# Kernel tuning notes

Hardware: AMD Instinct MI355X
Metric: run time of the kernel (lower is better)

## Reference

```python
import jax, jax.numpy as jnp
import numpy as np

NUM_EVENTS = 8   # events per batch (equal-sized, so we can reshape [N] -> [B,E])
K = 16           # kNN neighbors (includes self, distance 0 -> weight 1)
LN_EPS = 1e-5


def setup_inputs() -> dict:
    key = jax.random.key(0)
    ks = jax.random.split(key, 4)
    N, D, S, P = 32768, 256, 4, 32
    x = jax.random.normal(ks[0], (N, D), jnp.float32)
    batch_index = jnp.repeat(jnp.arange(NUM_EVENTS, dtype=jnp.int32), N // NUM_EVENTS)
    def lin(k, fan_in, fan_out):
        return jax.random.normal(k, (fan_in, fan_out), jnp.float32) / np.sqrt(fan_in).astype(np.float32)
    Ws = lin(ks[1], D, S);            bs = jnp.zeros((S,), jnp.float32)
    Wh = lin(ks[2], D, P);            bh = jnp.zeros((P,), jnp.float32)
    Wo = lin(ks[3], D + 2 * P, D);    bo = jnp.zeros((D,), jnp.float32)
    gamma = jnp.ones((D,), jnp.float32)
    beta = jnp.zeros((D,), jnp.float32)
    return dict(x=x, batch_index=batch_index, Ws=Ws, bs=bs, Wh=Wh, bh=bh,
                Wo=Wo, bo=bo, gamma=gamma, beta=beta)


def reference(x, batch_index, Ws, bs, Wh, bh, Wo, bo, gamma, beta):
    # GravNetConv: learned-space kNN + distance-weighted mean/max aggregation,
    # followed by residual add + LayerNorm (dropout p=0, eval mode).
    N, D = x.shape
    B = NUM_EVENTS
    E = N // B                                   # equal-sized events (batch_index is block-sorted)
    s = (x @ Ws + bs).reshape(B, E, -1)          # [B,E,S] learned coordinates
    h = (x @ Wh + bh).reshape(B, E, -1)          # [B,E,P] propagated features
    # per-event squared distances [B,E,E]; S=4 so this is traffic-bound
    d2 = jnp.sum((s[:, :, None, :] - s[:, None, :, :]) ** 2, axis=-1)
    neg_d2_k, idx = jax.lax.top_k(-d2, K)        # k smallest distances; idx [B,E,K]
    w = jnp.exp(10.0 * neg_d2_k)                 # edge_weight = exp(-10 * d^2), [B,E,K]
    h_nb = jax.vmap(lambda hb, ib: hb[ib])(h, idx)   # gather neighbor feats [B,E,K,P]
    msg = h_nb * w[..., None]                    # weighted messages
    agg_mean = jnp.mean(msg, axis=2)             # [B,E,P]
    agg_max = jnp.max(msg, axis=2)               # [B,E,P]
    xb = x.reshape(B, E, D)
    x_new = jnp.concatenate([xb, agg_mean, agg_max], axis=-1) @ Wo + bo  # lin_out
    # residual + LayerNorm
    y = xb + x_new
    mu = jnp.mean(y, axis=-1, keepdims=True)
    var = jnp.mean((y - mu) ** 2, axis=-1, keepdims=True)
    y = gamma * (y - mu) * jax.lax.rsqrt(var + LN_EPS) + beta
    return y.reshape(N, D)
```

## Files before the change

### kernel.cpp

```cpp
#include <hip/hip_runtime.h>
#include <stdint.h>

typedef short short8 __attribute__((ext_vector_type(8)));
typedef float f32x4 __attribute__((ext_vector_type(4)));
typedef unsigned short u16;

#define N_TOT 32768
#define EV 4096

__device__ __forceinline__ u16 f2bf(float f){
  unsigned int x = __float_as_uint(f);
  x += 0x7FFFu + ((x >> 16) & 1u);
  return (u16)(x >> 16);
}
__device__ __forceinline__ unsigned umin_(unsigned a, unsigned b){ return a<b?a:b; }

__global__ __launch_bounds__(256, 3) void kA(
    const float* __restrict__ x, const float* __restrict__ Ws,
    const float* __restrict__ bs, const float* __restrict__ Wh,
    const float* __restrict__ bh, const float* __restrict__ Wo,
    float* __restrict__ sOut, uint4* __restrict__ sfrag,
    unsigned short* __restrict__ hOut, unsigned int* __restrict__ WoT2)
{
  if (blockIdx.x >= N_TOT/64){
    const int kb = (blockIdx.x - N_TOT/64) * 32;
    const int c = threadIdx.x;
    unsigned int prev = 0;
    for (int k=0;k<32;++k){
      float v = Wo[(size_t)(kb+k)*256 + c];
      u16 h = f2bf(v);
      if (k & 1) WoT2[(size_t)c*160 + ((kb+k)>>1)] = prev | ((unsigned)h<<16);
      else       prev = (unsigned)h;
    }
    return;
  }
  __shared__ u16 xh[64*264];
  __shared__ u16 whT[32*264];
  const int t = threadIdx.x;
  const int wv = t >> 6, l = t & 63;
  const int r0 = blockIdx.x * 64;

  #pragma unroll
  for (int i=0;i<32;++i){
    int k = i*8 + (t>>5);
    int col = t & 31;
    whT[col*264 + k] = f2bf(Wh[(size_t)k*32 + col]);
  }

  {
    const int row = t >> 2, c40 = t & 3;
    const float4* xr = (const float4*)(x + (size_t)(r0+row)*256);
    const float4* wsr = (const float4*)Ws;
    float a0=0.f,a1=0.f,a2=0.f,a3=0.f;
    #pragma unroll
    for (int i=0;i<16;++i){
      int c4 = c40 + i*4;
      float4 xv = xr[c4];
      unsigned p0,p1;
      asm("v_cvt_pk_bf16_f32 %0, %1, %2" : "=v"(p0) : "v"(xv.x), "v"(xv.y));
      asm("v_cvt_pk_bf16_f32 %0, %1, %2" : "=v"(p1) : "v"(xv.z), "v"(xv.w));
      uint2 pk = {p0, p1};
      *(uint2*)&xh[row*264 + c4*4] = pk;
      float4 w0 = wsr[c4*4+0], w1 = wsr[c4*4+1], w2 = wsr[c4*4+2], w3 = wsr[c4*4+3];
      a0 += xv.x*w0.x + xv.y*w1.x + xv.z*w2.x + xv.w*w3.x;
      a1 += xv.x*w0.y + xv.y*w1.y + xv.z*w2.y + xv.w*w3.y;
      a2 += xv.x*w0.z + xv.y*w1.z + xv.z*w2.z + xv.w*w3.z;
      a3 += xv.x*w0.w + xv.y*w1.w + xv.z*w2.w + xv.w*w3.w;
    }
    a0 += __shfl_xor(a0,1); a0 += __shfl_xor(a0,2);
    a1 += __shfl_xor(a1,1); a1 += __shfl_xor(a1,2);
    a2 += __shfl_xor(a2,1); a2 += __shfl_xor(a2,2);
    a3 += __shfl_xor(a3,1); a3 += __shfl_xor(a3,2);
    if (c40 == 0){
      float4 sv = { a0+bs[0], a1+bs[1], a2+bs[2], a3+bs[3] };
      ((float4*)sOut)[r0 + row] = sv;
      u16 h0=f2bf(sv.x), h1=f2bf(sv.y), h2=f2bf(sv.z), h3=f2bf(sv.w);
      float e0 = sv.x - __uint_as_float((unsigned)h0<<16);
      float e1 = sv.y - __uint_as_float((unsigned)h1<<16);
      float e2 = sv.z - __uint_as_float((unsigned)h2<<16);
      float e3 = sv.w - __uint_as_float((unsigned)h3<<16);
      u16 l0=f2bf(e0), l1=f2bf(e1), l2=f2bf(e2), l3=f2bf(e3);
      float n = sv.x*sv.x + sv.y*sv.y + sv.z*sv.z + sv.w*sv.w;
      u16 nh = f2bf(n);
      u16 nl = f2bf(n - __uint_as_float((unsigned)nh<<16));
      uint4 w0, w1;
      w0.x = (unsigned)h0 | ((unsigned)h1<<16);
      w0.y = (unsigned)h2 | ((unsigned)h3<<16);
      w0.z = w0.x; w0.w = w0.y;
      w1.x = (unsigned)l0 | ((unsigned)l1<<16);
      w1.y = (unsigned)l2 | ((unsigned)l3<<16);
      w1.z = (unsigned)nh | ((unsigned)nl<<16);
      w1.w = 0x3F803F80u;
      sfrag[(size_t)(r0+row)*2 + 0] = w0;
      sfrag[(size_t)(r0+row)*2 + 1] = w1;
    }
  }
  __syncthreads();

  {
    const int lq = l & 15, g = l >> 4;
    const f32x4 zero = {0.f,0.f,0.f,0.f};
    f32x4 h0 = zero, h1 = zero;
    #pragma unroll
    for (int ks=0; ks<8; ++ks){
      short8 a  = *(const short8*)&xh[(wv*16+lq)*264 + ks*32 + g*8];
      short8 b0 = *(const short8*)&whT[lq*264       + ks*32 + g*8];
      short8 b1 = *(const short8*)&whT[(16+lq)*264  + ks*32 + g*8];
      h0 = __builtin_amdgcn_mfma_f32_16x16x32_bf16(a, b0, h0, 0,0,0);
      h1 = __builtin_amdgcn_mfma_f32_16x16x32_bf16(a, b1, h1, 0,0,0);
    }
    float bv0 = bh[lq], bv1 = bh[16+lq];
    #pragma unroll
    for (int rg=0; rg<4; ++rg){
      int rowg = r0 + wv*16 + g*4 + rg;
      hOut[(size_t)rowg*32 + lq]      = f2bf(h0[rg] + bv0);
      hOut[(size_t)rowg*32 + 16 + lq] = f2bf(h1[rg] + bv1);
    }
  }
}

#define BUBBLE16(v)                                              \
  { _Pragma("unroll")                                            \
    for (int k=0;k<16;++k){                                      \
      unsigned int mn = (v) < bp[k] ? (v) : bp[k];               \
      unsigned int mx = (v) < bp[k] ? bp[k] : (v);               \
      bp[k] = mn; (v) = mx;                                      \
    } }

#define MERGE16(OT)                                              \
  { unsigned int c[16];                                          \
    _Pragma("unroll")                                            \
    for (int k=0;k<16;++k){ unsigned int b2 = (OT)[15-k];        \
      c[k] = bp[k] < b2 ? bp[k] : b2; }                          \
    _Pragma("unroll")                                            \
    for (int d=8; d>=1; d>>=1){                                  \
      _Pragma("unroll")                                          \
      for (int i=0;i<16;++i){                                    \
        if ((i & d) == 0){                                       \
          unsigned int lo = c[i] < c[i+d] ? c[i] : c[i+d];       \
          unsigned int hi = c[i] < c[i+d] ? c[i+d] : c[i];       \
          c[i] = lo; c[i+d] = hi;                                \
        }                                                        \
      }                                                          \
    }                                                            \
    _Pragma("unroll")                                            \
    for (int k=0;k<16;++k) bp[k] = c[k]; }

#define SCAP 448
#define BIN_LO 440u

#define P1BODY(F, TL)                                            \
  { union { uint4 q; short8 v; } au; au.q = (F);                 \
    if (ld) (F) = fw[(size_t)((TL)+4)*32 + a32];                 \
    f32x4 acc = __builtin_amdgcn_mfma_f32_16x16x32_bf16(au.v, bq, zacc, 0,0,0); \
    _Pragma("unroll")                                            \
    for (int rg=0; rg<4; ++rg){                                  \
      unsigned u = __float_as_uint(fmaxf(acc[rg],0.f));          \
      unsigned q21 = u >> 21;                                    \
      unsigned b = (q21 < BIN_LO) ? 0u : umin_(q21 - BIN_LO, 127u); \
      atomicAdd(&hist[hbase + (b>>1)], (b&1u) ? 0x10000u : 1u);  \
    } }

#define P2BODY(F, TL)                                            \
  { union { uint4 q; short8 v; } au; au.q = (F);                 \
    if (ld) (F) = fw[(size_t)((TL)+4)*32 + a32];                 \
    f32x4 acc = __builtin_amdgcn_mfma_f32_16x16x32_bf16(au.v, bq, zacc, 0,0,0); \
    const int jb = jt + (TL)*16;                                 \
    _Pragma("unroll")                                            \
    for (int rg=0; rg<4; ++rg){                                  \
      int u = (int)__float_as_uint(acc[rg]);                     \
      if (u < tauS){                                             \
        unsigned idx = atomicAdd(&scnt[q16], 1u);                \
        if (idx < (unsigned)SCAP) slist[q16*SCAP + idx] = (u16)(jb + rg); \
      }                                                          \
    } }

__global__ __launch_bounds__(256, 8) void kB(
    const float* __restrict__ sIn, const uint4* __restrict__ sfrag,
    const unsigned short* __restrict__ hIn, unsigned short* __restrict__ Umini)
{
  __shared__ unsigned int hist[16*65];
  __shared__ u16 slist[16*SCAP];
  __shared__ unsigned int scnt[16];
  __shared__ unsigned int tauL[16];
  __shared__ unsigned int mrg[48][17];
  const int t = threadIdx.x;
  const int wv = t >> 6, l = t & 63;
  const int e = blockIdx.x >> 8;
  const int qblk = (blockIdx.x & 255) * 16;
  const int q16 = l & 15, g = l >> 4;
  const int qloc = qblk + q16;

  const float4* sg = (const float4*)sIn;
  const float4 sq = sg[(size_t)e*EV + qloc];
  const float si2 = sq.x*sq.x + sq.y*sq.y + sq.z*sq.z + sq.w*sq.w;

  union BU { u16 u[8]; short8 v; } bu;
  #pragma unroll
  for (int i2=0;i2<8;++i2) bu.u[i2]=0;
  {
    float tx=-2.f*sq.x, ty=-2.f*sq.y, tz=-2.f*sq.z, tw=-2.f*sq.w;
    u16 h0=f2bf(tx), h1=f2bf(ty), h2=f2bf(tz), h3=f2bf(tw);
    if (g==0){
      float e0 = tx - __uint_as_float((unsigned)h0<<16);
      float e1 = ty - __uint_as_float((unsigned)h1<<16);
      float e2 = tz - __uint_as_float((unsigned)h2<<16);
      float e3 = tw - __uint_as_float((unsigned)h3<<16);
      bu.u[0]=h0; bu.u[1]=h1; bu.u[2]=h2; bu.u[3]=h3;
      bu.u[4]=f2bf(e0); bu.u[5]=f2bf(e1); bu.u[6]=f2bf(e2); bu.u[7]=f2bf(e3);
    } else if (g==1){
      u16 sh = f2bf(si2);
      u16 sl = f2bf(si2 - __uint_as_float((unsigned)sh<<16));
      bu.u[0]=h0; bu.u[1]=h1; bu.u[2]=h2; bu.u[3]=h3;
      bu.u[4]=0x3F80; bu.u[5]=0x3F80; bu.u[6]=sh; bu.u[7]=sl;
    }
  }
  const short8 bq = bu.v;

  for (int i=t; i<16*65; i+=256) hist[i]=0;
  if (t < 16) scnt[t] = 0;
  __syncthreads();

  const f32x4 zacc = {0.f,0.f,0.f,0.f};
  const uint4 zf4 = {0,0,0,0};
  const uint4* fw = sfrag + (((size_t)e*EV + wv*1024) << 1);
  const int a32 = q16*2 + g;
  const bool ld = (l < 32);
  const int hbase = q16*65;

  {
    uint4 f0 = ld ? fw[a32]      : zf4;
    uint4 f1 = ld ? fw[32 + a32] : zf4;
    uint4 f2 = ld ? fw[64 + a32] : zf4;
    uint4 f3 = ld ? fw[96 + a32] : zf4;
    for (int tl=0; tl<16; tl+=4){
      P1BODY(f0, tl+0)
      P1BODY(f1, tl+1)
      P1BODY(f2, tl+2)
      P1BODY(f3, tl+3)
    }
  }
  __syncthreads();

  {
    int q = t >> 4, i = t & 15;
    int base = q*65 + i*4;
    unsigned w0=hist[base], w1=hist[base+1], w2=hist[base+2], w3=hist[base+3];
    unsigned cnt[8] = { w0&0xFFFFu, w0>>16, w1&0xFFFFu, w1>>16,
                        w2&0xFFFFu, w2>>16, w3&0xFFFFu, w3>>16 };
    unsigned cs = 0;
    #pragma unroll
    for (int k2=0;k2<8;++k2) cs += cnt[k2];
    unsigned ps = cs;
    #pragma unroll
    for (int d=1; d<16; d<<=1){
      unsigned o = __shfl_up(ps, d, 16);
      if ((t&15) >= d) ps += o;
    }
    if (ps >= 16u && (ps - cs) < 16u){
      unsigned run = ps - cs;
      unsigned B = 127;
      #pragma unroll
      for (int k2=0;k2<8;++k2){
        unsigned c2 = cnt[k2];
        bool hit = (run < 16u) && (run + c2 >= 16u);
        if (hit) B = (unsigned)(i*8 + k2);
        run += c2;
      }
      tauL[q] = (B >= 127u) ? 0x7F800001u : ((BIN_LO + B + 1u) << 21);
    }
  }
  __syncthreads();
  const int tauS = (int)tauL[q16];

  {
    uint4 f0 = ld ? fw[a32]      : zf4;
    uint4 f1 = ld ? fw[32 + a32] : zf4;
    uint4 f2 = ld ? fw[64 + a32] : zf4;
    uint4 f3 = ld ? fw[96 + a32] : zf4;
    const int jt = wv*1024 + g*4;
    for (int tl=0; tl<64; tl+=4){
      P2BODY(f0, tl+0)
      P2BODY(f1, tl+1)
      P2BODY(f2, tl+2)
      P2BODY(f3, tl+3)
    }
  }
  __syncthreads();

  unsigned scn_raw = scnt[q16];
  unsigned int bp[16];
  #pragma unroll
  for (int k=0;k<16;++k) bp[k]=0xFFFFFFFFu;
  const int lane16 = wv*4 + g;
  if (scn_raw > (unsigned)SCAP){
    for (int jj=lane16; jj<EV; jj+=16){
      float4 s4 = sg[(size_t)e*EV + jj];
      float dx = sq.x-s4.x, dy = sq.y-s4.y, dz = sq.z-s4.z, dw = sq.w-s4.w;
      float d2 = dx*dx + dy*dy + dz*dz + dw*dw;
      unsigned key = (__float_as_uint(d2) & 0xFFFFF000u) | (unsigned)jj;
      if (key < bp[15]) { BUBBLE16(key) }
    }
  } else {
    for (unsigned i=lane16; i<scn_raw; i+=16){
      int jj = (int)slist[q16*SCAP + i];
      float4 s4 = sg[(size_t)e*EV + jj];
      float dx = sq.x-s4.x, dy = sq.y-s4.y, dz = sq.z-s4.z, dw = sq.w-s4.w;
      float d2 = dx*dx + dy*dy + dz*dz + dw*dw;
      unsigned key = (__float_as_uint(d2) & 0xFFFFF000u) | (unsigned)jj;
      BUBBLE16(key)
    }
  }

  #pragma unroll
  for (int st=0; st<2; ++st){
    const int msk = (st==0) ? 16 : 32;
    unsigned int ot[16];
    #pragma unroll
    for (int k=0;k<16;++k) ot[k] = (unsigned int)__shfl_xor((int)bp[k], msk, 64);
    MERGE16(ot)
  }

  if (wv != 0 && l < 16){
    #pragma unroll
    for (int k=0;k<16;++k) mrg[(wv-1)*16 + l][k] = bp[k];
  }
  __syncthreads();
  if (wv != 0) return;
  #pragma unroll
  for (int w=0; w<3; ++w){
    unsigned int ot[16];
    #pragma unroll
    for (int k=0;k<16;++k) ot[k] = mrg[w*16 + q16][k];
    MERGE16(ot)
  }

  float am[8], ax[8];
  #pragma unroll
  for (int p=0;p<8;++p){ am[p]=0.f; ax[p]=-3.4e38f; }
  const uint4* hb = (const uint4*)(hIn + (size_t)e*EV*32);
  #pragma unroll
  for (int i=0;i<16;++i){
    unsigned int key = bp[i];
    int j = (int)(key & 0xFFFu);
    float d2 = __uint_as_float(key & 0xFFFFF000u);
    float w = __expf(-10.f * d2);
    uint4 hv = hb[(size_t)j*4 + g];
    unsigned int uu[4] = {hv.x, hv.y, hv.z, hv.w};
    #pragma unroll
    for (int c2=0;c2<4;++c2){
      float flo = __uint_as_float(uu[c2] << 16);
      float fhi = __uint_as_float(uu[c2] & 0xFFFF0000u);
      float m0 = w*flo, m1 = w*fhi;
      am[c2*2]   += m0;                 am[c2*2+1] += m1;
      ax[c2*2]    = fmaxf(ax[c2*2],m0); ax[c2*2+1]  = fmaxf(ax[c2*2+1],m1);
    }
  }
  {
    unsigned short* Ur = Umini + ((size_t)e*EV + qloc)*64;
    uint4 pm, px;
    pm.x = (unsigned)f2bf(am[0]*(1.f/16.f)) | ((unsigned)f2bf(am[1]*(1.f/16.f))<<16);
    pm.y = (unsigned)f2bf(am[2]*(1.f/16.f)) | ((unsigned)f2bf(am[3]*(1.f/16.f))<<16);
    pm.z = (unsigned)f2bf(am[4]*(1.f/16.f)) | ((unsigned)f2bf(am[5]*(1.f/16.f))<<16);
    pm.w = (unsigned)f2bf(am[6]*(1.f/16.f)) | ((unsigned)f2bf(am[7]*(1.f/16.f))<<16);
    px.x = (unsigned)f2bf(ax[0]) | ((unsigned)f2bf(ax[1])<<16);
    px.y = (unsigned)f2bf(ax[2]) | ((unsigned)f2bf(ax[3])<<16);
    px.z = (unsigned)f2bf(ax[4]) | ((unsigned)f2bf(ax[5])<<16);
    px.w = (unsigned)f2bf(ax[6]) | ((unsigned)f2bf(ax[7])<<16);
    *(uint4*)(Ur +  0 + g*8) = pm;
    *(uint4*)(Ur + 32 + g*8) = px;
  }
}

__global__ __launch_bounds__(256, 4) void kC(
    const unsigned short* __restrict__ Umini, const unsigned short* __restrict__ WoT,
    const float* __restrict__ bo, const float* __restrict__ x,
    const float* __restrict__ gamma, const float* __restrict__ beta,
    float* __restrict__ out)
{
  __shared__ unsigned short At[64*40];
  __shared__ unsigned short Bt[256*40];
  __shared__ float ps[64*4], pq[64*4];
  const int t = threadIdx.x;
  const int r0 = blockIdx.x * 64;
  const int l = t & 63, wv = t >> 6;
  const int lq = l & 15, g = l >> 4;
  f32x4 acc[4][4];
  const f32x4 zero = {0.f,0.f,0.f,0.f};
  #pragma unroll
  for (int m=0;m<4;++m)
    #pragma unroll
    for (int n=0;n<4;++n) acc[m][n] = zero;

  for (int kk=0; kk<10; ++kk){
    const int k0 = kk*32;
    __syncthreads();
    {
      int row = t >> 2, ko = (t & 3)*8;
      uint4 av;
      if (k0 < 256){
        const float4* xr = (const float4*)(x + (size_t)(r0+row)*256 + k0 + ko);
        float4 u0 = xr[0], u1 = xr[1];
        unsigned p0,p1,p2,p3;
        asm("v_cvt_pk_bf16_f32 %0, %1, %2" : "=v"(p0) : "v"(u0.x), "v"(u0.y));
        asm("v_cvt_pk_bf16_f32 %0, %1, %2" : "=v"(p1) : "v"(u0.z), "v"(u0.w));
        asm("v_cvt_pk_bf16_f32 %0, %1, %2" : "=v"(p2) : "v"(u1.x), "v"(u1.y));
        asm("v_cvt_pk_bf16_f32 %0, %1, %2" : "=v"(p3) : "v"(u1.z), "v"(u1.w));
        av.x = p0; av.y = p1; av.z = p2; av.w = p3;
      } else {
        av = *(const uint4*)(Umini + (size_t)(r0+row)*64 + (k0-256) + ko);
      }
      *(uint4*)(At + row*40 + ko) = av;
    }
    {
      int col = t;
      const uint4* src = (const uint4*)(WoT + (size_t)col*320 + k0);
      #pragma unroll
      for (int j=0;j<4;++j) *(uint4*)(Bt + col*40 + j*8) = src[j];
    }
    __syncthreads();
    short8 a[4], b[4];
    #pragma unroll
    for (int m=0;m<4;++m) a[m] = *(const short8*)(At + (16*m+lq)*40 + g*8);
    #pragma unroll
    for (int n=0;n<4;++n) b[n] = *(const short8*)(Bt + (wv*64 + 16*n + lq)*40 + g*8);
    #pragma unroll
    for (int m=0;m<4;++m)
      #pragma unroll
      for (int n=0;n<4;++n)
        acc[m][n] = __builtin_amdgcn_mfma_f32_16x16x32_bf16(a[m], b[n], acc[m][n], 0, 0, 0);
  }

  float bo_n[4], ga_n[4], be_n[4];
  #pragma unroll
  for (int n=0;n<4;++n){
    int colg = wv*64 + 16*n + lq;
    bo_n[n] = bo[colg]; ga_n[n] = gamma[colg]; be_n[n] = beta[colg];
  }
  float pr[4][4], pr2[4][4];
  #pragma unroll
  for (int m=0;m<4;++m){
    #pragma unroll
    for (int rg=0;rg<4;++rg){
      int rowg = r0 + 16*m + g*4 + rg;
      float sum=0.f, sq=0.f;
      #pragma unroll
      for (int n=0;n<4;++n){
        int colg = wv*64 + 16*n + lq;
        float y = acc[m][n][rg] + bo_n[n] + x[(size_t)rowg*256 + colg];
        acc[m][n][rg] = y;
        sum += y; sq += y*y;
      }
      sum += __shfl_xor(sum,1); sq += __shfl_xor(sq,1);
      sum += __shfl_xor(sum,2); sq += __shfl_xor(sq,2);
      sum += __shfl_xor(sum,4); sq += __shfl_xor(sq,4);
      sum += __shfl_xor(sum,8); sq += __shfl_xor(sq,8);
      pr[m][rg]=sum; pr2[m][rg]=sq;
    }
  }
  if (lq == 0){
    #pragma unroll
    for (int m=0;m<4;++m)
      #pragma unroll
      for (int rg=0;rg<4;++rg){
        int rowl = 16*m + g*4 + rg;
        ps[rowl*4 + wv] = pr[m][rg];
        pq[rowl*4 + wv] = pr2[m][rg];
      }
  }
  __syncthreads();
  #pragma unroll
  for (int m=0;m<4;++m){
    #pragma unroll
    for (int rg=0;rg<4;++rg){
      int rowl = 16*m + g*4 + rg;
      float sum = ps[rowl*4+0]+ps[rowl*4+1]+ps[rowl*4+2]+ps[rowl*4+3];
      float sq  = pq[rowl*4+0]+pq[rowl*4+1]+pq[rowl*4+2]+pq[rowl*4+3];
      float mu  = sum * (1.f/256.f);
      float var = sq * (1.f/256.f) - mu*mu;
      float inv = rsqrtf(var + 1e-5f);
      int rowg = r0 + rowl;
      #pragma unroll
      for (int n=0;n<4;++n){
        int colg = wv*64 + 16*n + lq;
        out[(size_t)rowg*256 + colg] = ga_n[n]*(acc[m][n][rg] - mu)*inv + be_n[n];
      }
    }
  }
}

extern "C" void kernel_launch(void* const* d_in, const int* in_sizes, int n_in,
                              void* d_out, int out_size, void* d_ws, size_t ws_size,
                              hipStream_t stream)
{
  const float* x     = (const float*)d_in[0];
  const float* Ws    = (const float*)d_in[2];
  const float* bs    = (const float*)d_in[3];
  const float* Wh    = (const float*)d_in[4];
  const float* bh    = (const float*)d_in[5];
  const float* Wo    = (const float*)d_in[6];
  const float* bo    = (const float*)d_in[7];
  const float* gamma = (const float*)d_in[8];
  const float* beta  = (const float*)d_in[9];
  float* out = (float*)d_out;

  char* ws = (char*)d_ws;
  float*          sBuf  = (float*)ws;
  uint4*          sfrag = (uint4*)(ws + 524288);
  unsigned short* hBuf  = (unsigned short*)(ws + 1572864);
  unsigned short* Umini = (unsigned short*)(ws + 3670016);
  unsigned short* WoT   = (unsigned short*)(ws + 7864320);

  kA<<<dim3(N_TOT/64 + 10), dim3(256), 0, stream>>>(x, Ws, bs, Wh, bh, Wo,
                                                    sBuf, sfrag, hBuf, (unsigned int*)WoT);
  kB<<<dim3(N_TOT/16), dim3(256), 0, stream>>>(sBuf, sfrag, hBuf, Umini);
  kC<<<dim3(N_TOT/64), dim3(256), 0, stream>>>(Umini, WoT, bo, x, gamma, beta, out);
}
```

Baseline: 133.5 us.

## Switch kNN distance MFMA to 32x32x16 tiles, 32 queries per block

Kernel kB now computes the distance tiles with the 32x32x16 bf16 MFMA instead of 16x16x32. Each block covers 32 queries, and all 64 lanes load fragments, where before only half the lanes did. Candidate refinement moves to two waves that each scan the whole candidate list for 16 queries, which removes the cross-wave merge through shared memory. In exchange, per-block LDS grows, occupancy drops to 4 blocks, the launch has half as many blocks, and the tail runs with fewer active waves.

```diff
diff --git a/kernel.cpp b/kernel.cpp
--- a/kernel.cpp
+++ b/kernel.cpp
@@ -3,6 +3,7 @@
 
 typedef short short8 __attribute__((ext_vector_type(8)));
 typedef float f32x4 __attribute__((ext_vector_type(4)));
+typedef float f32x16 __attribute__((ext_vector_type(16)));
 typedef unsigned short u16;
 
 #define N_TOT 32768
@@ -151,10 +152,10 @@
 
 #define P1BODY(F, TL)                                            \
   { union { uint4 q; short8 v; } au; au.q = (F);                 \
-    if (ld) (F) = fw[(size_t)((TL)+4)*32 + a32];                 \
-    f32x4 acc = __builtin_amdgcn_mfma_f32_16x16x32_bf16(au.v, bq, zacc, 0,0,0); \
+    (F) = fw[(size_t)((TL)+4)*64 + a64];                         \
+    f32x16 acc = __builtin_amdgcn_mfma_f32_32x32x16_bf16(au.v, bq, zacc, 0,0,0); \
     _Pragma("unroll")                                            \
-    for (int rg=0; rg<4; ++rg){                                  \
+    for (int rg=0; rg<16; ++rg){                                 \
       unsigned u = __float_as_uint(fmaxf(acc[rg],0.f));          \
       unsigned q21 = u >> 21;                                    \
       unsigned b = (q21 < BIN_LO) ? 0u : umin_(q21 - BIN_LO, 127u); \
@@ -163,77 +164,72 @@
 
 #define P2BODY(F, TL)                                            \
   { union { uint4 q; short8 v; } au; au.q = (F);                 \
-    if (ld) (F) = fw[(size_t)((TL)+4)*32 + a32];                 \
-    f32x4 acc = __builtin_amdgcn_mfma_f32_16x16x32_bf16(au.v, bq, zacc, 0,0,0); \
-    const int jb = jt + (TL)*16;                                 \
+    (F) = fw[(size_t)((TL)+4)*64 + a64];                         \
+    f32x16 acc = __builtin_amdgcn_mfma_f32_32x32x16_bf16(au.v, bq, zacc, 0,0,0); \
+    const int jb2 = jb + (TL)*32;                                \
     _Pragma("unroll")                                            \
-    for (int rg=0; rg<4; ++rg){                                  \
+    for (int rg=0; rg<16; ++rg){                                 \
       int u = (int)__float_as_uint(acc[rg]);                     \
       if (u < tauS){                                             \
-        unsigned idx = atomicAdd(&scnt[q16], 1u);                \
-        if (idx < (unsigned)SCAP) slist[q16*SCAP + idx] = (u16)(jb + rg); \
+        int j = jb2 + (rg&3) + 8*(rg>>2);                        \
+        unsigned idx = atomicAdd(&scnt[q32], 1u);                \
+        if (idx < (unsigned)SCAP) slist[q32*SCAP + idx] = (u16)j; \
       }                                                          \
     } }
 
-__global__ __launch_bounds__(256, 8) void kB(
+__global__ __launch_bounds__(256, 4) void kB(
     const float* __restrict__ sIn, const uint4* __restrict__ sfrag,
     const unsigned short* __restrict__ hIn, unsigned short* __restrict__ Umini)
 {
-  __shared__ unsigned int hist[16*65];
-  __shared__ u16 slist[16*SCAP];
-  __shared__ unsigned int scnt[16];
-  __shared__ unsigned int tauL[16];
-  __shared__ unsigned int mrg[48][17];
+  __shared__ unsigned int hist[32*65];
+  __shared__ u16 slist[32*SCAP];
+  __shared__ unsigned int scnt[32];
+  __shared__ unsigned int tauL[32];
   const int t = threadIdx.x;
   const int wv = t >> 6, l = t & 63;
-  const int e = blockIdx.x >> 8;
-  const int qblk = (blockIdx.x & 255) * 16;
-  const int q16 = l & 15, g = l >> 4;
-  const int qloc = qblk + q16;
+  const int e = blockIdx.x >> 7;
+  const int qblk = (blockIdx.x & 127) * 32;
+  const int q32 = l & 31, hi = l >> 5;
+  const int qloc = qblk + q32;
 
   const float4* sg = (const float4*)sIn;
   const float4 sq = sg[(size_t)e*EV + qloc];
   const float si2 = sq.x*sq.x + sq.y*sq.y + sq.z*sq.z + sq.w*sq.w;
 
   union BU { u16 u[8]; short8 v; } bu;
-  #pragma unroll
-  for (int i2=0;i2<8;++i2) bu.u[i2]=0;
   {
     float tx=-2.f*sq.x, ty=-2.f*sq.y, tz=-2.f*sq.z, tw=-2.f*sq.w;
     u16 h0=f2bf(tx), h1=f2bf(ty), h2=f2bf(tz), h3=f2bf(tw);
-    if (g==0){
+    bu.u[0]=h0; bu.u[1]=h1; bu.u[2]=h2; bu.u[3]=h3;
+    if (hi==0){
       float e0 = tx - __uint_as_float((unsigned)h0<<16);
       float e1 = ty - __uint_as_float((unsigned)h1<<16);
       float e2 = tz - __uint_as_float((unsigned)h2<<16);
       float e3 = tw - __uint_as_float((unsigned)h3<<16);
-      bu.u[0]=h0; bu.u[1]=h1; bu.u[2]=h2; bu.u[3]=h3;
       bu.u[4]=f2bf(e0); bu.u[5]=f2bf(e1); bu.u[6]=f2bf(e2); bu.u[7]=f2bf(e3);
-    } else if (g==1){
+    } else {
       u16 sh = f2bf(si2);
       u16 sl = f2bf(si2 - __uint_as_float((unsigned)sh<<16));
-      bu.u[0]=h0; bu.u[1]=h1; bu.u[2]=h2; bu.u[3]=h3;
       bu.u[4]=0x3F80; bu.u[5]=0x3F80; bu.u[6]=sh; bu.u[7]=sl;
     }
   }
   const short8 bq = bu.v;
 
-  for (int i=t; i<16*65; i+=256) hist[i]=0;
-  if (t < 16) scnt[t] = 0;
+  for (int i=t; i<32*65; i+=256) hist[i]=0;
+  if (t < 32) scnt[t] = 0;
   __syncthreads();
 
-  const f32x4 zacc = {0.f,0.f,0.f,0.f};
-  const uint4 zf4 = {0,0,0,0};
+  const f32x16 zacc = {0.f,0.f,0.f,0.f,0.f,0.f,0.f,0.f,0.f,0.f,0.f,0.f,0.f,0.f,0.f,0.f};
   const uint4* fw = sfrag + (((size_t)e*EV + wv*1024) << 1);
-  const int a32 = q16*2 + g;
-  const bool ld = (l < 32);
-  const int hbase = q16*65;
-
-  {
-    uint4 f0 = ld ? fw[a32]      : zf4;
-    uint4 f1 = ld ? fw[32 + a32] : zf4;
-    uint4 f2 = ld ? fw[64 + a32] : zf4;
-    uint4 f3 = ld ? fw[96 + a32] : zf4;
-    for (int tl=0; tl<16; tl+=4){
+  const int a64 = q32*2 + hi;
+  const int hbase = q32*65;
+
+  {
+    uint4 f0 = fw[a64];
+    uint4 f1 = fw[64  + a64];
+    uint4 f2 = fw[128 + a64];
+    uint4 f3 = fw[192 + a64];
+    for (int tl=0; tl<8; tl+=4){
       P1BODY(f0, tl+0)
       P1BODY(f1, tl+1)
       P1BODY(f2, tl+2)
@@ -243,43 +239,47 @@
   __syncthreads();
 
   {
-    int q = t >> 4, i = t & 15;
-    int base = q*65 + i*4;
-    unsigned w0=hist[base], w1=hist[base+1], w2=hist[base+2], w3=hist[base+3];
-    unsigned cnt[8] = { w0&0xFFFFu, w0>>16, w1&0xFFFFu, w1>>16,
-                        w2&0xFFFFu, w2>>16, w3&0xFFFFu, w3>>16 };
+    int q = t >> 3, i = t & 7;
+    int base = q*65 + i*8;
+    unsigned cnt[16];
+    #pragma unroll
+    for (int w2=0; w2<8; ++w2){
+      unsigned w = hist[base + w2];
+      cnt[w2*2]   = w & 0xFFFFu;
+      cnt[w2*2+1] = w >> 16;
+    }
     unsigned cs = 0;
     #pragma unroll
-    for (int k2=0;k2<8;++k2) cs += cnt[k2];
+    for (int k2=0;k2<16;++k2) cs += cnt[k2];
     unsigned ps = cs;
     #pragma unroll
-    for (int d=1; d<16; d<<=1){
-      unsigned o = __shfl_up(ps, d, 16);
-      if ((t&15) >= d) ps += o;
+    for (int d=1; d<8; d<<=1){
+      unsigned o = __shfl_up(ps, d, 8);
+      if ((t&7) >= d) ps += o;
     }
     if (ps >= 16u && (ps - cs) < 16u){
       unsigned run = ps - cs;
       unsigned B = 127;
       #pragma unroll
-      for (int k2=0;k2<8;++k2){
+      for (int k2=0;k2<16;++k2){
         unsigned c2 = cnt[k2];
         bool hit = (run < 16u) && (run + c2 >= 16u);
-        if (hit) B = (unsigned)(i*8 + k2);
+        if (hit) B = (unsigned)(i*16 + k2);
         run += c2;
       }
       tauL[q] = (B >= 127u) ? 0x7F800001u : ((BIN_LO + B + 1u) << 21);
     }
   }
   __syncthreads();
-  const int tauS = (int)tauL[q16];
-
-  {
-    uint4 f0 = ld ? fw[a32]      : zf4;
-    uint4 f1 = ld ? fw[32 + a32] : zf4;
-    uint4 f2 = ld ? fw[64 + a32] : zf4;
-    uint4 f3 = ld ? fw[96 + a32] : zf4;
-    const int jt = wv*1024 + g*4;
-    for (int tl=0; tl<64; tl+=4){
+  const int tauS = (int)tauL[q32];
+
+  {
+    uint4 f0 = fw[a64];
+    uint4 f1 = fw[64  + a64];
+    uint4 f2 = fw[128 + a64];
+    uint4 f3 = fw[192 + a64];
+    const int jb = wv*1024 + 4*hi;
+    for (int tl=0; tl<32; tl+=4){
       P2BODY(f0, tl+0)
       P2BODY(f1, tl+1)
       P2BODY(f2, tl+2)
@@ -287,25 +287,29 @@
     }
   }
   __syncthreads();
-
-  unsigned scn_raw = scnt[q16];
+  if (wv >= 2) return;
+
+  const int q16 = l & 15, g = l >> 4;
+  const int qq = wv*16 + q16;
+  const int qlocf = qblk + qq;
+  const float4 sqf = sg[(size_t)e*EV + qlocf];
+  unsigned scn_raw = scnt[qq];
   unsigned int bp[16];
   #pragma unroll
   for (int k=0;k<16;++k) bp[k]=0xFFFFFFFFu;
-  const int lane16 = wv*4 + g;
   if (scn_raw > (unsigned)SCAP){
-    for (int jj=lane16; jj<EV; jj+=16){
+    for (int jj=g; jj<EV; jj+=4){
       float4 s4 = sg[(size_t)e*EV + jj];
-      float dx = sq.x-s4.x, dy = sq.y-s4.y, dz = sq.z-s4.z, dw = sq.w-s4.w;
+      float dx = sqf.x-s4.x, dy = sqf.y-s4.y, dz = sqf.z-s4.z, dw = sqf.w-s4.w;
       float d2 = dx*dx + dy*dy + dz*dz + dw*dw;
       unsigned key = (__float_as_uint(d2) & 0xFFFFF000u) | (unsigned)jj;
       if (key < bp[15]) { BUBBLE16(key) }
     }
   } else {
-    for (unsigned i=lane16; i<scn_raw; i+=16){
-      int jj = (int)slist[q16*SCAP + i];
+    for (unsigned i=g; i<scn_raw; i+=4){
+      int jj = (int)slist[qq*SCAP + i];
       float4 s4 = sg[(size_t)e*EV + jj];
-      float dx = sq.x-s4.x, dy = sq.y-s4.y, dz = sq.z-s4.z, dw = sq.w-s4.w;
+      float dx = sqf.x-s4.x, dy = sqf.y-s4.y, dz = sqf.z-s4.z, dw = sqf.w-s4.w;
       float d2 = dx*dx + dy*dy + dz*dz + dw*dw;
       unsigned key = (__float_as_uint(d2) & 0xFFFFF000u) | (unsigned)jj;
       BUBBLE16(key)
@@ -318,20 +322,6 @@
     unsigned int ot[16];
     #pragma unroll
     for (int k=0;k<16;++k) ot[k] = (unsigned int)__shfl_xor((int)bp[k], msk, 64);
-    MERGE16(ot)
-  }
-
-  if (wv != 0 && l < 16){
-    #pragma unroll
-    for (int k=0;k<16;++k) mrg[(wv-1)*16 + l][k] = bp[k];
-  }
-  __syncthreads();
-  if (wv != 0) return;
-  #pragma unroll
-  for (int w=0; w<3; ++w){
-    unsigned int ot[16];
-    #pragma unroll
-    for (int k=0;k<16;++k) ot[k] = mrg[w*16 + q16][k];
     MERGE16(ot)
   }
 
@@ -357,7 +347,7 @@
     }
   }
   {
-    unsigned short* Ur = Umini + ((size_t)e*EV + qloc)*64;
+    unsigned short* Ur = Umini + ((size_t)e*EV + qlocf)*64;
     uint4 pm, px;
     pm.x = (unsigned)f2bf(am[0]*(1.f/16.f)) | ((unsigned)f2bf(am[1]*(1.f/16.f))<<16);
     pm.y = (unsigned)f2bf(am[2]*(1.f/16.f)) | ((unsigned)f2bf(am[3]*(1.f/16.f))<<16);
@@ -513,6 +503,6 @@
 
   kA<<<dim3(N_TOT/64 + 10), dim3(256), 0, stream>>>(x, Ws, bs, Wh, bh, Wo,
                                                     sBuf, sfrag, hBuf, (unsigned int*)WoT);
-  kB<<<dim3(N_TOT/16), dim3(256), 0, stream>>>(sBuf, sfrag, hBuf, Umini);
+  kB<<<dim3(N_TOT/32), dim3(256), 0, stream>>>(sBuf, sfrag, hBuf, Umini);
   kC<<<dim3(N_TOT/64), dim3(256), 0, stream>>>(Umini, WoT, bo, x, gamma, beta, out);
 }
```

New measurement: 131.5 us. About the same (-1.5%).
